# Kernel tuning notes

Measured on AMD Instinct MI355X. Metric: run time of the kernel, lower is better.

The kernel has to match this reference:

```python
import jax, jax.numpy as jnp
import numpy as np

B_, S_, H_, I_, N_, K_ = 2, 2048, 1024, 2048, 16, 4

def setup_inputs() -> dict:
    key = jax.random.key(0)
    ks = jax.random.split(key, 6)
    return {
        "x": jax.random.normal(ks[0], (B_, S_, H_), jnp.float32),
        "W_in": jax.random.normal(ks[1], (H_, 2 * I_), jnp.float32) * (H_ ** -0.5),
        "conv_w": jax.random.normal(ks[2], (I_, 1, K_), jnp.float32) * (K_ ** -0.5),
        "ln_gamma": jnp.ones((I_,), jnp.float32),
        "ln_beta": jnp.zeros((I_,), jnp.float32),
        "W_xproj": jax.random.normal(ks[3], (I_, 2 * N_ + 1), jnp.float32) * (I_ ** -0.5),
        "A_param": jax.random.normal(ks[4], (I_, N_), jnp.float32) * 0.1,
        "D": jnp.ones((I_,), jnp.float32),
        "W_out": jax.random.normal(ks[5], (I_, H_), jnp.float32) * (I_ ** -0.5),
    }

def _layernorm(x, g, b, eps=1e-5):
    mu = jnp.mean(x, axis=-1, keepdims=True)
    var = jnp.mean((x - mu) ** 2, axis=-1, keepdims=True)
    return (x - mu) * jax.lax.rsqrt(var + eps) * g + b

def reference(x, W_in, conv_w, ln_gamma, ln_beta, W_xproj, A_param, D, W_out):
    b, s, _ = x.shape
    n = A_param.shape[1]
    xz = x @ W_in                                   # (b,s,2I)
    xc, z = jnp.split(xz, 2, axis=-1)
    # depthwise causal conv1d: torch pads both sides k-1 then truncates [:s] == left-pad k-1
    xc = jax.lax.conv_general_dilated(
        xc.transpose(0, 2, 1), conv_w, window_strides=(1,),
        padding=[(conv_w.shape[-1] - 1, 0)],
        feature_group_count=conv_w.shape[0],
        dimension_numbers=("NCH", "OIH", "NCH")).transpose(0, 2, 1)  # (b,s,I)
    xc = jax.nn.silu(xc)
    xc = _layernorm(xc, ln_gamma, ln_beta)
    xp = xc @ W_xproj                               # (b,s,2N+1)
    delta = jnp.clip(jax.nn.softplus(xp[..., :1]), 1e-6, 10.0)   # (b,s,1)
    Bm = xp[..., 1:1 + n]                           # (b,s,N)
    Cm = xp[..., 1 + n:]                            # (b,s,N)
    A = -jnp.clip(jax.nn.softplus(A_param), 0.1, 10.0)           # (I,N)
    # decay[b,s,i,n] = exp(delta[b,s] * A[i,n]), clamped
    decay = jnp.clip(jnp.exp(delta[..., None] * A[None, None]), 1e-6, 1.0)  # (b,s,I,N)
    # y = x * sum_n B*C*decay  (state-dim reduction of the broadcast 4D tensor)
    y = xc * jnp.einsum("bsn,bsin->bsi", Bm * Cm, decay)
    y = y + xc * D
    return (y * jax.nn.silu(z)) @ W_out
```

## Files before the change

kernel.cpp:

```cpp
#include <hip/hip_runtime.h>
#include <hip/hip_bf16.h>
#include <cmath>

typedef __bf16 bf16_t;
typedef __bf16 bf16x8 __attribute__((ext_vector_type(8)));
typedef __bf16 bf16x4 __attribute__((ext_vector_type(4)));
typedef float  f32x4  __attribute__((ext_vector_type(4)));

static constexpr int B_  = 2, S_ = 2048, H_ = 1024, I_ = 2048, NST = 16;
static constexpr int ROWS  = B_ * S_;
static constexpr int TWO_I = 2 * I_;
static constexpr int XPD   = 2 * NST + 1;
static constexpr int XPN   = 64;

#define AS_G(p) ((const __attribute__((address_space(1))) void*)(p))
#define AS_L(p) ((__attribute__((address_space(3))) void*)(p))

template<int N> __device__ __forceinline__ void wait_vmcnt();
template<> __device__ __forceinline__ void wait_vmcnt<4>() {
    asm volatile("s_waitcnt vmcnt(4)" ::: "memory");
}

__device__ __forceinline__ float softplus_f(float x) {
    return x > 15.f ? x : log1pf(__expf(x));
}

__device__ __forceinline__ f32x4 b2f(bf16x4 v) {
    return (f32x4){(float)v[0], (float)v[1], (float)v[2], (float)v[3]};
}

__device__ __forceinline__ float fast_exp2(float x) {
#if __has_builtin(__builtin_amdgcn_exp2f)
    return __builtin_amdgcn_exp2f(x);
#else
    return exp2f(x);
#endif
}
__device__ __forceinline__ float fast_rcp(float x) {
#if __has_builtin(__builtin_amdgcn_rcpf)
    return __builtin_amdgcn_rcpf(x);
#else
    return 1.f / x;
#endif
}
__device__ __forceinline__ float fast_sigmoid(float x) {
    return fast_rcp(1.f + __expf(-x));
}
__device__ __forceinline__ float rflf(float x) {
    return __int_as_float(__builtin_amdgcn_readfirstlane(__float_as_int(x)));
}

template<int GX, int GY, int XW>
__device__ __forceinline__ void xcd_swz(int id, int& bx, int& by) {
    constexpr int SX = GX / XW;
    constexpr int SY = GY * XW / 8;
    const int xcd = id & 7;
    const int j   = id >> 3;
    bx = (xcd % XW) * SX + j % SX;
    by = (xcd / XW) * SY + j / SX;
}


__global__ __launch_bounds__(256)
void prep_all(const float* __restrict__ x, const float* __restrict__ W_in,
              const float* __restrict__ W_out, const float* __restrict__ A_param,
              const float* __restrict__ Wx, const float* __restrict__ conv_w,
              bf16_t* __restrict__ Xb, bf16_t* __restrict__ W1t,
              bf16_t* __restrict__ Wot, float* __restrict__ A2T,
              float* __restrict__ cwT, bf16_t* __restrict__ WxTb)
{
    const int b   = blockIdx.x;
    const int tid = threadIdx.x;
    __shared__ float t[32][33];

    if (b < 4096) {
        const int i = b * 256 + tid;
        f32x4 v = *(const f32x4*)(x + (size_t)i * 4);
        bf16x4 o;
        o[0] = (bf16_t)v[0]; o[1] = (bf16_t)v[1];
        o[2] = (bf16_t)v[2]; o[3] = (bf16_t)v[3];
        *(bf16x4*)(Xb + (size_t)i * 4) = o;
    } else if (b < 8192) {
        const int tb = b - 4096;
        const int c0 = (tb & 127) * 32, r0 = (tb >> 7) * 32;
        const int tx = tid & 31, ty = tid >> 5;
        #pragma unroll
        for (int k = 0; k < 4; ++k)
            t[ty + 8 * k][tx] = W_in[(size_t)(r0 + ty + 8 * k) * 4096 + c0 + tx];
        __syncthreads();
        #pragma unroll
        for (int k = 0; k < 4; ++k)
            W1t[(size_t)(c0 + ty + 8 * k) * 1024 + r0 + tx] = (bf16_t)t[tx][ty + 8 * k];
    } else if (b < 10240) {
        const int tb = b - 8192;
        const int c0 = (tb & 31) * 32, r0 = (tb >> 5) * 32;
        const int tx = tid & 31, ty = tid >> 5;
        #pragma unroll
        for (int k = 0; k < 4; ++k)
            t[ty + 8 * k][tx] = W_out[(size_t)(r0 + ty + 8 * k) * 1024 + c0 + tx];
        __syncthreads();
        #pragma unroll
        for (int k = 0; k < 4; ++k)
            Wot[(size_t)(c0 + ty + 8 * k) * 2048 + r0 + tx] = (bf16_t)t[tx][ty + 8 * k];
    } else {
        const int i = (b - 10240) * 256 + tid;
        if (i < NST * I_) {
            int n = i >> 11, c = i & (I_ - 1);
            float sp = softplus_f(A_param[(size_t)c * NST + n]);
            A2T[i] = -fminf(fmaxf(sp, 0.1f), 10.f) * 1.44269504088896340736f;
        }
        if (i < 4 * I_) {
            int j = i >> 11, c = i & (I_ - 1);
            cwT[i] = conv_w[(size_t)c * 4 + j];
        }
        if (i < XPN * I_) {
            int j = i >> 11, c = i & (I_ - 1);
            WxTb[i] = (j < XPD) ? (bf16_t)Wx[(size_t)c * XPD + j] : (bf16_t)0.f;
        }
    }
}


template<int M, int N, int K, int BM, int BN, int WM, int WN, int THREADS,
         int GX, int GY, int XW, typename OutT>
__global__ __launch_bounds__(THREADS)
void gemm_fp(const bf16_t* __restrict__ A, const bf16_t* __restrict__ Bt,
             OutT* __restrict__ C)
{
    constexpr int BK  = 32;
    constexpr int NT  = K / BK;
    constexpr int MR  = BM / WM / 16;
    constexpr int NR  = BN / WN / 16;
    constexpr int MH  = MR / 2;
    constexpr int RPC = THREADS / 4;
    constexpr int CA  = BM / RPC;
    constexpr int CB  = BN / RPC;
    static_assert(CA + CB == 4, "vmcnt template fixed at 4");

    __shared__ bf16_t lA[4][BM * BK];
    __shared__ bf16_t lB[4][BN * BK];

    int bx, by;
    xcd_swz<GX, GY, XW>(blockIdx.x, bx, by);
    const int bm = by * BM;
    const int bn = bx * BN;

    const int tid  = threadIdx.x;
    const int lane = tid & 63;
    const int wave = tid >> 6;
    const int wm   = wave / WN;
    const int wn   = wave % WN;

    const int frow = lane & 15;
    const int fsw  = ((lane >> 4) ^ ((frow >> 1) & 3)) << 3;

    const int str = tid >> 2;
    const int stp = tid & 3;

    const bf16_t* baseA[CA];
    #pragma unroll
    for (int a = 0; a < CA; ++a) {
        const int rt = a * RPC + str;
        baseA[a] = A + (size_t)(bm + rt) * K + ((stp ^ ((rt >> 1) & 3)) << 3);
    }
    const bf16_t* baseB[CB];
    #pragma unroll
    for (int a = 0; a < CB; ++a) {
        const int rt = a * RPC + str;
        baseB[a] = Bt + (size_t)(bn + rt) * K + ((stp ^ ((rt >> 1) & 3)) << 3);
    }

    f32x4 acc[MR][NR];
    #pragma unroll
    for (int m = 0; m < MR; ++m)
        #pragma unroll
        for (int n = 0; n < NR; ++n)
            acc[m][n] = (f32x4){0.f, 0.f, 0.f, 0.f};

    auto stageA = [&](int k0, int b) {
        #pragma unroll
        for (int a = 0; a < CA; ++a)
            __builtin_amdgcn_global_load_lds(AS_G(baseA[a] + k0),
                AS_L(&lA[b][a * RPC * 32 + wave * 512]), 16, 0, 0);
    };
    auto stageB = [&](int k0, int b) {
        #pragma unroll
        for (int a = 0; a < CB; ++a)
            __builtin_amdgcn_global_load_lds(AS_G(baseB[a] + k0),
                AS_L(&lB[b][a * RPC * 32 + wave * 512]), 16, 0, 0);
    };

    stageA(0, 0); stageB(0, 0);
    stageA(BK, 1); stageB(BK, 1);
    wait_vmcnt<4>();
    __builtin_amdgcn_s_barrier();

    #pragma unroll 1
    for (int t = 0; t < NT; ++t) {
        const int buf = t & 3;
        const int nb  = (t + 2) & 3;
        int kn = (t + 2) * BK;
        if (kn >= K) kn -= K;

        bf16x8 bfr[NR];
        #pragma unroll
        for (int n = 0; n < NR; ++n)
            bfr[n] = *(const bf16x8*)(&lB[buf][(wn * (NR * 16) + n * 16 + frow) * 32 + fsw]);
        bf16x8 af0[MH];
        #pragma unroll
        for (int m = 0; m < MH; ++m)
            af0[m] = *(const bf16x8*)(&lA[buf][(wm * (MR * 16) + m * 16 + frow) * 32 + fsw]);
        stageA(kn, nb);

        __builtin_amdgcn_s_setprio(1);
        #pragma unroll
        for (int m = 0; m < MH; ++m)
            #pragma unroll
            for (int n = 0; n < NR; ++n)
                acc[m][n] = __builtin_amdgcn_mfma_f32_16x16x32_bf16(
                    af0[m], bfr[n], acc[m][n], 0, 0, 0);
        __builtin_amdgcn_s_setprio(0);

        bf16x8 af1[MR - MH];
        #pragma unroll
        for (int m = 0; m < MR - MH; ++m)
            af1[m] = *(const bf16x8*)(&lA[buf][(wm * (MR * 16) + (MH + m) * 16 + frow) * 32 + fsw]);
        stageB(kn, nb);

        __builtin_amdgcn_s_setprio(1);
        #pragma unroll
        for (int m = 0; m < MR - MH; ++m)
            #pragma unroll
            for (int n = 0; n < NR; ++n)
                acc[MH + m][n] = __builtin_amdgcn_mfma_f32_16x16x32_bf16(
                    af1[m], bfr[n], acc[MH + m][n], 0, 0, 0);
        __builtin_amdgcn_s_setprio(0);

        wait_vmcnt<4>();
        __builtin_amdgcn_s_barrier();
    }

    const int crow = (lane >> 4) * 4;
    const int ccol = lane & 15;
    #pragma unroll
    for (int m = 0; m < MR; ++m)
        #pragma unroll
        for (int n = 0; n < NR; ++n)
            #pragma unroll
            for (int r = 0; r < 4; ++r)
                C[(size_t)(bm + wm * (MR * 16) + m * 16 + crow + r) * N
                  + (bn + wn * (NR * 16) + n * 16 + ccol)] = (OutT)acc[m][n][r];
}


template<int M, int N, int K, int GX, int GY, int XW>
__global__ __launch_bounds__(512)
void gemm3_kg(const bf16_t* __restrict__ A, const bf16_t* __restrict__ Bt,
              float* __restrict__ C)
{
    constexpr int BM = 128, BN = 128, BK = 32;
    constexpr int KH = K / 2;
    constexpr int NT = KH / BK;
    constexpr int MR = 4, NR = 4, MH = 2;

    __shared__ bf16_t smem[65536];

    int bx, by;
    xcd_swz<GX, GY, XW>(blockIdx.x, bx, by);
    const int bm = by * BM;
    const int bn = bx * BN;

    const int tid  = threadIdx.x;
    const int lane = tid & 63;
    const int wave = tid >> 6;
    const int grp  = wave >> 2;
    const int gw   = wave & 3;
    const int wm   = gw >> 1;
    const int wn   = gw & 1;

    const int frow = lane & 15;
    const int fsw  = ((lane >> 4) ^ ((frow >> 1) & 3)) << 3;

    const int gtid = tid & 255;
    const int str  = gtid >> 2;
    const int stp  = gtid & 3;

    bf16_t* lA = smem + grp * 16384;
    bf16_t* lB = smem + 32768 + grp * 16384;

    const bf16_t* baseA[2];
    #pragma unroll
    for (int a = 0; a < 2; ++a) {
        const int rt = a * 64 + str;
        baseA[a] = A + (size_t)(bm + rt) * K + grp * KH + ((stp ^ ((rt >> 1) & 3)) << 3);
    }
    const bf16_t* baseB[2];
    #pragma unroll
    for (int a = 0; a < 2; ++a) {
        const int rt = a * 64 + str;
        baseB[a] = Bt + (size_t)(bn + rt) * K + grp * KH + ((stp ^ ((rt >> 1) & 3)) << 3);
    }

    f32x4 acc[MR][NR];
    #pragma unroll
    for (int m = 0; m < MR; ++m)
        #pragma unroll
        for (int n = 0; n < NR; ++n)
            acc[m][n] = (f32x4){0.f, 0.f, 0.f, 0.f};

    auto stageA = [&](int k0, int b) {
        #pragma unroll
        for (int a = 0; a < 2; ++a)
            __builtin_amdgcn_global_load_lds(AS_G(baseA[a] + k0),
                AS_L(lA + b * 4096 + a * 2048 + gw * 512), 16, 0, 0);
    };
    auto stageB = [&](int k0, int b) {
        #pragma unroll
        for (int a = 0; a < 2; ++a)
            __builtin_amdgcn_global_load_lds(AS_G(baseB[a] + k0),
                AS_L(lB + b * 4096 + a * 2048 + gw * 512), 16, 0, 0);
    };

    stageA(0, 0); stageB(0, 0);
    stageA(BK, 1); stageB(BK, 1);
    wait_vmcnt<4>();
    __builtin_amdgcn_s_barrier();

    #pragma unroll 1
    for (int t = 0; t < NT; ++t) {
        const int buf = t & 3;
        const int nb  = (t + 2) & 3;
        int kn = (t + 2) * BK;
        if (kn >= KH) kn -= KH;

        bf16x8 bfr[NR];
        #pragma unroll
        for (int n = 0; n < NR; ++n)
            bfr[n] = *(const bf16x8*)(lB + buf * 4096 + (wn * 64 + n * 16 + frow) * 32 + fsw);
        bf16x8 af0[MH];
        #pragma unroll
        for (int m = 0; m < MH; ++m)
            af0[m] = *(const bf16x8*)(lA + buf * 4096 + (wm * 64 + m * 16 + frow) * 32 + fsw);
        stageA(kn, nb);

        __builtin_amdgcn_s_setprio(1);
        #pragma unroll
        for (int m = 0; m < MH; ++m)
            #pragma unroll
            for (int n = 0; n < NR; ++n)
                acc[m][n] = __builtin_amdgcn_mfma_f32_16x16x32_bf16(
                    af0[m], bfr[n], acc[m][n], 0, 0, 0);
        __builtin_amdgcn_s_setprio(0);

        bf16x8 af1[MR - MH];
        #pragma unroll
        for (int m = 0; m < MR - MH; ++m)
            af1[m] = *(const bf16x8*)(lA + buf * 4096 + (wm * 64 + (MH + m) * 16 + frow) * 32 + fsw);
        stageB(kn, nb);

        __builtin_amdgcn_s_setprio(1);
        #pragma unroll
        for (int m = 0; m < MR - MH; ++m)
            #pragma unroll
            for (int n = 0; n < NR; ++n)
                acc[MH + m][n] = __builtin_amdgcn_mfma_f32_16x16x32_bf16(
                    af1[m], bfr[n], acc[MH + m][n], 0, 0, 0);
        __builtin_amdgcn_s_setprio(0);

        wait_vmcnt<4>();
        __builtin_amdgcn_s_barrier();
    }

    asm volatile("s_waitcnt vmcnt(0)" ::: "memory");
    __builtin_amdgcn_s_barrier();

    float* accx = (float*)smem;
    const int crow = (lane >> 4) * 4;
    const int ccol = lane & 15;

    if (grp == 1) {
        #pragma unroll
        for (int m = 0; m < MR; ++m)
            #pragma unroll
            for (int n = 0; n < NR; ++n) {
                const int row = wm * 64 + m * 16 + crow;
                const int col = wn * 64 + n * 16 + ccol;
                #pragma unroll
                for (int r = 0; r < 4; ++r)
                    accx[(size_t)(row + r) * 132 + col] = acc[m][n][r];
            }
    }
    __syncthreads();
    if (grp == 0) {
        #pragma unroll
        for (int m = 0; m < MR; ++m)
            #pragma unroll
            for (int n = 0; n < NR; ++n) {
                const int row = wm * 64 + m * 16 + crow;
                const int col = wn * 64 + n * 16 + ccol;
                #pragma unroll
                for (int r = 0; r < 4; ++r)
                    C[(size_t)(bm + row + r) * N + bn + col] =
                        acc[m][n][r] + accx[(size_t)(row + r) * 132 + col];
            }
    }
}


__global__ __launch_bounds__(256)
void conv_ln(const bf16_t* __restrict__ xz,
             const float* __restrict__ cwT,
             const float* __restrict__ ln_g,
             const float* __restrict__ ln_b,
             bf16_t* __restrict__ Xn)
{
    const int row  = blockIdx.x;
    const int s    = row & (S_ - 1);
    const int tid  = threadIdx.x;
    const int lane = tid & 63;
    const int wave = tid >> 6;
    const bf16_t* xzr = xz + (size_t)row * TWO_I;

    __shared__ float lnr[4][2];

    float xc[8];
    float sm = 0.f, sq = 0.f;

    #pragma unroll
    for (int g = 0; g < 2; ++g) {
        const int c = g * 1024 + tid * 4;
        const f32x4 w0 = *(const f32x4*)(cwT + 0 * I_ + c);
        const f32x4 w1 = *(const f32x4*)(cwT + 1 * I_ + c);
        const f32x4 w2 = *(const f32x4*)(cwT + 2 * I_ + c);
        const f32x4 w3 = *(const f32x4*)(cwT + 3 * I_ + c);
        const f32x4 z4 = (f32x4){0.f, 0.f, 0.f, 0.f};
        const f32x4 xv0 = (s >= 3) ? b2f(*(const bf16x4*)(xzr - 3 * TWO_I + c)) : z4;
        const f32x4 xv1 = (s >= 2) ? b2f(*(const bf16x4*)(xzr - 2 * TWO_I + c)) : z4;
        const f32x4 xv2 = (s >= 1) ? b2f(*(const bf16x4*)(xzr - 1 * TWO_I + c)) : z4;
        const f32x4 xv3 = b2f(*(const bf16x4*)(xzr + c));
        const f32x4 a = w0 * xv0 + w1 * xv1 + w2 * xv2 + w3 * xv3;
        #pragma unroll
        for (int e = 0; e < 4; ++e) {
            const float v = a[e];
            const float t = v * fast_sigmoid(v);
            xc[g * 4 + e] = t;
            sm += t; sq += t * t;
        }
    }

    #pragma unroll
    for (int off = 32; off; off >>= 1) {
        sm += __shfl_xor(sm, off, 64);
        sq += __shfl_xor(sq, off, 64);
    }
    if (lane == 0) { lnr[wave][0] = sm; lnr[wave][1] = sq; }
    __syncthreads();
    sm = lnr[0][0] + lnr[1][0] + lnr[2][0] + lnr[3][0];
    sq = lnr[0][1] + lnr[1][1] + lnr[2][1] + lnr[3][1];
    const float mu = sm * (1.f / I_);
    const float rs = rsqrtf(sq * (1.f / I_) - mu * mu + 1e-5f);

    #pragma unroll
    for (int g = 0; g < 2; ++g) {
        const int c = g * 1024 + tid * 4;
        const f32x4 gg = *(const f32x4*)(ln_g + c);
        const f32x4 bb = *(const f32x4*)(ln_b + c);
        bf16x4 h4;
        #pragma unroll
        for (int e = 0; e < 4; ++e)
            h4[e] = (bf16_t)((xc[g * 4 + e] - mu) * rs * gg[e] + bb[e]);
        *(bf16x4*)(Xn + (size_t)row * I_ + c) = h4;
    }
}


__global__ __launch_bounds__(256)
void xproj_gemm(const bf16_t* __restrict__ Xn,
                const bf16_t* __restrict__ Wb, float* __restrict__ xp_part)
{
    constexpr int BM = 128, BK = 32, KS = 512;
    __shared__ bf16_t lA[BM * BK];
    __shared__ bf16_t lB[XPN * BK];

    const int bm   = blockIdx.x * BM;
    const int ks   = blockIdx.y;
    const int tid  = threadIdx.x;
    const int lane = tid & 63;
    const int wave = tid >> 6;
    const int wm   = (wave >> 1) * 64;
    const int wn   = (wave & 1) * 32;

    const int srow  = lane >> 2;
    const int skoff = (lane & 3) * 8;
    const int frow  = lane & 15;
    const int fko   = (lane >> 4) * 8;

    f32x4 acc[4][2];
    #pragma unroll
    for (int m = 0; m < 4; ++m)
        #pragma unroll
        for (int n = 0; n < 2; ++n)
            acc[m][n] = (f32x4){0.f, 0.f, 0.f, 0.f};

    for (int k0 = ks * KS; k0 < ks * KS + KS; k0 += BK) {
        #pragma unroll
        for (int t = 0; t < 2; ++t) {
            const int c = wave * 2 + t;
            const bf16_t* ga = Xn + (size_t)(bm + c * 16 + srow) * I_ + k0 + skoff;
            __builtin_amdgcn_global_load_lds(AS_G(ga), AS_L(lA + c * 512), 16, 0, 0);
        }
        const bf16_t* gb = Wb + (size_t)(wave * 16 + srow) * I_ + k0 + skoff;
        __builtin_amdgcn_global_load_lds(AS_G(gb), AS_L(lB + wave * 512), 16, 0, 0);
        __syncthreads();

        bf16x8 af[4], bf2[2];
        #pragma unroll
        for (int m = 0; m < 4; ++m)
            af[m] = *(const bf16x8*)(lA + (wm + m * 16 + frow) * BK + fko);
        #pragma unroll
        for (int n = 0; n < 2; ++n)
            bf2[n] = *(const bf16x8*)(lB + (wn + n * 16 + frow) * BK + fko);

        #pragma unroll
        for (int m = 0; m < 4; ++m)
            #pragma unroll
            for (int n = 0; n < 2; ++n)
                acc[m][n] = __builtin_amdgcn_mfma_f32_16x16x32_bf16(
                    af[m], bf2[n], acc[m][n], 0, 0, 0);

        __syncthreads();
    }

    float* out = xp_part + ((size_t)ks * ROWS + bm) * XPN;
    const int crow = (lane >> 4) * 4;
    const int ccol = lane & 15;
    #pragma unroll
    for (int m = 0; m < 4; ++m)
        #pragma unroll
        for (int n = 0; n < 2; ++n)
            #pragma unroll
            for (int r = 0; r < 4; ++r)
                out[(size_t)(wm + m * 16 + crow + r) * XPN
                    + (wn + n * 16 + ccol)] = acc[m][n][r];
}


__global__ __launch_bounds__(256)
void ssm_gate(const bf16_t* __restrict__ xz,
              const bf16_t* __restrict__ Xn,
              const float* __restrict__ xp_part,
              const float* __restrict__ A2T,
              const float* __restrict__ Dv,
              bf16_t* __restrict__ U)
{
    const int row0 = blockIdx.x * 2;
    const int tid  = threadIdx.x;

    __shared__ float xps[2][XPD];
    __shared__ float bcs[2][NST];

    if (tid < XPD) {
        float s = 0.f;
        #pragma unroll
        for (int ks = 0; ks < 4; ++ks)
            s += xp_part[((size_t)ks * ROWS + row0) * XPN + tid];
        xps[0][tid] = s;
    } else if (tid >= 64 && tid < 64 + XPD) {
        const int j = tid - 64;
        float s = 0.f;
        #pragma unroll
        for (int ks = 0; ks < 4; ++ks)
            s += xp_part[((size_t)ks * ROWS + row0 + 1) * XPN + j];
        xps[1][j] = s;
    }
    __syncthreads();
    if (tid < NST)
        bcs[0][tid] = xps[0][1 + tid] * xps[0][1 + NST + tid];
    else if (tid >= 64 && tid < 64 + NST) {
        const int n = tid - 64;
        bcs[1][n] = xps[1][1 + n] * xps[1][1 + NST + n];
    }
    __syncthreads();

    const float d0 = fminf(fmaxf(softplus_f(xps[0][0]), 1e-6f), 10.f);
    const float d1 = fminf(fmaxf(softplus_f(xps[1][0]), 1e-6f), 10.f);

    const bf16_t* z0 = xz + (size_t)row0 * TWO_I + I_;
    const bf16_t* z1 = z0 + TWO_I;
    bf16_t* u0 = U + (size_t)row0 * I_;
    bf16_t* u1 = u0 + I_;

    #pragma unroll 1
    for (int g = 0; g < 2; ++g) {
        const int c = g * 1024 + tid * 4;
        f32x4 sa0 = (f32x4){0.f, 0.f, 0.f, 0.f};
        f32x4 sa1 = (f32x4){0.f, 0.f, 0.f, 0.f};
        #pragma unroll 1
        for (int nb = 0; nb < 4; ++nb) {
            const float* ap = A2T + (size_t)(nb * 4) * I_ + c;
            const f32x4 a0 = *(const f32x4*)(ap);
            const f32x4 a1 = *(const f32x4*)(ap + I_);
            const f32x4 a2 = *(const f32x4*)(ap + 2 * I_);
            const f32x4 a3 = *(const f32x4*)(ap + 3 * I_);
            const float b00 = rflf(bcs[0][nb * 4 + 0]), b10 = rflf(bcs[1][nb * 4 + 0]);
            const float b01 = rflf(bcs[0][nb * 4 + 1]), b11 = rflf(bcs[1][nb * 4 + 1]);
            const float b02 = rflf(bcs[0][nb * 4 + 2]), b12 = rflf(bcs[1][nb * 4 + 2]);
            const float b03 = rflf(bcs[0][nb * 4 + 3]), b13 = rflf(bcs[1][nb * 4 + 3]);
            #pragma unroll
            for (int e = 0; e < 4; ++e) {
                sa0[e] += b00 * fast_exp2(d0 * a0[e]);
                sa1[e] += b10 * fast_exp2(d1 * a0[e]);
                sa0[e] += b01 * fast_exp2(d0 * a1[e]);
                sa1[e] += b11 * fast_exp2(d1 * a1[e]);
                sa0[e] += b02 * fast_exp2(d0 * a2[e]);
                sa1[e] += b12 * fast_exp2(d1 * a2[e]);
                sa0[e] += b03 * fast_exp2(d0 * a3[e]);
                sa1[e] += b13 * fast_exp2(d1 * a3[e]);
            }
        }
        const f32x4 dvv = *(const f32x4*)(Dv + c);
        const f32x4 xn0 = b2f(*(const bf16x4*)(Xn + (size_t)row0 * I_ + c));
        const f32x4 xn1 = b2f(*(const bf16x4*)(Xn + (size_t)(row0 + 1) * I_ + c));
        const f32x4 zv0 = b2f(*(const bf16x4*)(z0 + c));
        const f32x4 zv1 = b2f(*(const bf16x4*)(z1 + c));
        bf16x4 o0, o1;
        #pragma unroll
        for (int e = 0; e < 4; ++e) {
            const float y0 = xn0[e] * (sa0[e] + dvv[e]);
            const float y1 = xn1[e] * (sa1[e] + dvv[e]);
            const float zz0 = zv0[e], zz1 = zv1[e];
            o0[e] = (bf16_t)(y0 * zz0 * fast_sigmoid(zz0));
            o1[e] = (bf16_t)(y1 * zz1 * fast_sigmoid(zz1));
        }
        *(bf16x4*)(u0 + c) = o0;
        *(bf16x4*)(u1 + c) = o1;
    }
}


extern "C" void kernel_launch(void* const* d_in, const int* in_sizes, int n_in,
                              void* d_out, int out_size, void* d_ws, size_t ws_size,
                              hipStream_t stream)
{
    const float* x     = (const float*)d_in[0];
    const float* W_in  = (const float*)d_in[1];
    const float* convw = (const float*)d_in[2];
    const float* ln_g  = (const float*)d_in[3];
    const float* ln_b  = (const float*)d_in[4];
    const float* Wx    = (const float*)d_in[5];
    const float* A_p   = (const float*)d_in[6];
    const float* Dv    = (const float*)d_in[7];
    const float* W_out = (const float*)d_in[8];
    float* out = (float*)d_out;

    char* ws = (char*)d_ws;
    bf16_t* Xb   = (bf16_t*)(ws);
    bf16_t* W1t  = (bf16_t*)(ws + (size_t)(8u  << 20));
    bf16_t* Wot  = (bf16_t*)(ws + (size_t)(16u << 20));
    float*  A2T  = (float*) (ws + (size_t)(20u << 20));
    float*  cwT  = (float*) (ws + (size_t)(20u << 20) + (128u << 10));
    bf16_t* WxTb = (bf16_t*)(ws + (size_t)(20u << 20) + (256u << 10));
    bf16_t* XZb  = (bf16_t*)(ws + (size_t)(22u << 20));
    bf16_t* U    = (bf16_t*)(ws + (size_t)(54u << 20));
    bf16_t* Xn   = (bf16_t*)(ws);
    float*  xp4  = (float*) (ws + (size_t)(86u << 20));

    prep_all<<<10752, 256, 0, stream>>>(x, W_in, W_out, A_p, Wx, convw,
                                        Xb, W1t, Wot, A2T, cwT, WxTb);

    gemm_fp<ROWS, TWO_I, H_, 256, 256, 2, 4, 512, 16, 16, 4, bf16_t>
        <<<256, 512, 0, stream>>>(Xb, W1t, XZb);
    conv_ln<<<ROWS, 256, 0, stream>>>(XZb, cwT, ln_g, ln_b, Xn);
    xproj_gemm<<<dim3(ROWS / 128, 4), 256, 0, stream>>>(Xn, WxTb, xp4);
    ssm_gate<<<ROWS / 2, 256, 0, stream>>>(XZb, Xn, xp4, A2T, Dv, U);
    gemm3_kg<ROWS, H_, I_, 8, 32, 2>
        <<<256, 512, 0, stream>>>(U, Wot, out);
}
```

Baseline: 125.0 us.

## Rewrite input GEMM with BK=64 double-buffered eight-phase MFMA schedule

Replaces the generic four-buffer BK=32 GEMM for the input projection with a specialized 256x256 tile kernel using BK=64, two LDS buffers and a row-XOR swizzle over eight 16-byte chunks. Each K-tile is split into four MFMA quadrants separated by barriers, with fragment loads and global-to-LDS staging interleaved between them, to overlap memory with compute and cut per-iteration loop overhead. The added barriers and larger per-wave fragment register footprint may reduce latency hiding or occupancy. There is also a risk of LDS overwrite hazards when staging into the buffer currently being read.

```diff
diff --git a/kernel.cpp b/kernel.cpp
--- a/kernel.cpp
+++ b/kernel.cpp
@@ -19,6 +19,9 @@
 template<int N> __device__ __forceinline__ void wait_vmcnt();
 template<> __device__ __forceinline__ void wait_vmcnt<4>() {
     asm volatile("s_waitcnt vmcnt(4)" ::: "memory");
+}
+template<> __device__ __forceinline__ void wait_vmcnt<8>() {
+    asm volatile("s_waitcnt vmcnt(8)" ::: "memory");
 }
 
 __device__ __forceinline__ float softplus_f(float x) {
@@ -121,24 +124,17 @@
 }
 
 
-template<int M, int N, int K, int BM, int BN, int WM, int WN, int THREADS,
-         int GX, int GY, int XW, typename OutT>
-__global__ __launch_bounds__(THREADS)
-void gemm_fp(const bf16_t* __restrict__ A, const bf16_t* __restrict__ Bt,
-             OutT* __restrict__ C)
+template<int M, int N, int K, int GX, int GY, int XW>
+__global__ __launch_bounds__(512)
+void gemm1_8p(const bf16_t* __restrict__ A, const bf16_t* __restrict__ Bt,
+              bf16_t* __restrict__ C)
 {
-    constexpr int BK  = 32;
-    constexpr int NT  = K / BK;
-    constexpr int MR  = BM / WM / 16;
-    constexpr int NR  = BN / WN / 16;
-    constexpr int MH  = MR / 2;
-    constexpr int RPC = THREADS / 4;
-    constexpr int CA  = BM / RPC;
-    constexpr int CB  = BN / RPC;
-    static_assert(CA + CB == 4, "vmcnt template fixed at 4");
-
-    __shared__ bf16_t lA[4][BM * BK];
-    __shared__ bf16_t lB[4][BN * BK];
+    constexpr int BM = 256, BN = 256, BK = 64;
+    constexpr int NKT = K / BK;
+    constexpr int NIT = NKT / 2;
+
+    __shared__ bf16_t lA[2 * 16384];
+    __shared__ bf16_t lB[2 * 16384];
 
     int bx, by;
     xcd_swz<GX, GY, XW>(blockIdx.x, bx, by);
@@ -148,108 +144,162 @@
     const int tid  = threadIdx.x;
     const int lane = tid & 63;
     const int wave = tid >> 6;
-    const int wm   = wave / WN;
-    const int wn   = wave % WN;
-
+    const int wm   = wave >> 2;
+    const int wn   = wave & 3;
     const int frow = lane & 15;
-    const int fsw  = ((lane >> 4) ^ ((frow >> 1) & 3)) << 3;
-
-    const int str = tid >> 2;
-    const int stp = tid & 3;
-
-    const bf16_t* baseA[CA];
-    #pragma unroll
-    for (int a = 0; a < CA; ++a) {
-        const int rt = a * RPC + str;
-        baseA[a] = A + (size_t)(bm + rt) * K + ((stp ^ ((rt >> 1) & 3)) << 3);
-    }
-    const bf16_t* baseB[CB];
-    #pragma unroll
-    for (int a = 0; a < CB; ++a) {
-        const int rt = a * RPC + str;
-        baseB[a] = Bt + (size_t)(bn + rt) * K + ((stp ^ ((rt >> 1) & 3)) << 3);
-    }
-
-    f32x4 acc[MR][NR];
-    #pragma unroll
-    for (int m = 0; m < MR; ++m)
-        #pragma unroll
-        for (int n = 0; n < NR; ++n)
+    const int ko   = lane >> 4;
+    const int fr7  = frow & 7;
+
+    const int str = tid >> 3;
+    const int stp = tid & 7;
+
+    const bf16_t* gA[4];
+    const bf16_t* gB[4];
+    #pragma unroll
+    for (int h = 0; h < 2; ++h)
+        #pragma unroll
+        for (int a = 0; a < 2; ++a) {
+            const int rt = h * 128 + a * 64 + str;
+            gA[h * 2 + a] = A  + (size_t)(bm + rt) * K + ((stp ^ (str & 7)) << 3);
+            gB[h * 2 + a] = Bt + (size_t)(bn + rt) * K + ((stp ^ (str & 7)) << 3);
+        }
+    const int ldst = wave * 512;
+
+    f32x4 acc[8][4];
+    #pragma unroll
+    for (int m = 0; m < 8; ++m)
+        #pragma unroll
+        for (int n = 0; n < 4; ++n)
             acc[m][n] = (f32x4){0.f, 0.f, 0.f, 0.f};
 
-    auto stageA = [&](int k0, int b) {
-        #pragma unroll
-        for (int a = 0; a < CA; ++a)
-            __builtin_amdgcn_global_load_lds(AS_G(baseA[a] + k0),
-                AS_L(&lA[b][a * RPC * 32 + wave * 512]), 16, 0, 0);
+    auto stageA2 = [&](int kt, int buf) {
+        #pragma unroll
+        for (int c = 0; c < 4; ++c)
+            __builtin_amdgcn_global_load_lds(AS_G(gA[c] + kt * BK),
+                AS_L(lA + buf * 16384 + c * 4096 + ldst), 16, 0, 0);
     };
-    auto stageB = [&](int k0, int b) {
-        #pragma unroll
-        for (int a = 0; a < CB; ++a)
-            __builtin_amdgcn_global_load_lds(AS_G(baseB[a] + k0),
-                AS_L(&lB[b][a * RPC * 32 + wave * 512]), 16, 0, 0);
+    auto stageB2 = [&](int kt, int buf) {
+        #pragma unroll
+        for (int c = 0; c < 4; ++c)
+            __builtin_amdgcn_global_load_lds(AS_G(gB[c] + kt * BK),
+                AS_L(lB + buf * 16384 + c * 4096 + ldst), 16, 0, 0);
     };
 
-    stageA(0, 0); stageB(0, 0);
-    stageA(BK, 1); stageB(BK, 1);
-    wait_vmcnt<4>();
+    stageA2(0, 0); stageB2(0, 0);
+    stageA2(1, 1); stageB2(1, 1);
+    wait_vmcnt<8>();
     __builtin_amdgcn_s_barrier();
 
     #pragma unroll 1
-    for (int t = 0; t < NT; ++t) {
-        const int buf = t & 3;
-        const int nb  = (t + 2) & 3;
-        int kn = (t + 2) * BK;
-        if (kn >= K) kn -= K;
-
-        bf16x8 bfr[NR];
-        #pragma unroll
-        for (int n = 0; n < NR; ++n)
-            bfr[n] = *(const bf16x8*)(&lB[buf][(wn * (NR * 16) + n * 16 + frow) * 32 + fsw]);
-        bf16x8 af0[MH];
-        #pragma unroll
-        for (int m = 0; m < MH; ++m)
-            af0[m] = *(const bf16x8*)(&lA[buf][(wm * (MR * 16) + m * 16 + frow) * 32 + fsw]);
-        stageA(kn, nb);
-
-        __builtin_amdgcn_s_setprio(1);
-        #pragma unroll
-        for (int m = 0; m < MH; ++m)
-            #pragma unroll
-            for (int n = 0; n < NR; ++n)
-                acc[m][n] = __builtin_amdgcn_mfma_f32_16x16x32_bf16(
-                    af0[m], bfr[n], acc[m][n], 0, 0, 0);
-        __builtin_amdgcn_s_setprio(0);
-
-        bf16x8 af1[MR - MH];
-        #pragma unroll
-        for (int m = 0; m < MR - MH; ++m)
-            af1[m] = *(const bf16x8*)(&lA[buf][(wm * (MR * 16) + (MH + m) * 16 + frow) * 32 + fsw]);
-        stageB(kn, nb);
-
-        __builtin_amdgcn_s_setprio(1);
-        #pragma unroll
-        for (int m = 0; m < MR - MH; ++m)
-            #pragma unroll
-            for (int n = 0; n < NR; ++n)
-                acc[MH + m][n] = __builtin_amdgcn_mfma_f32_16x16x32_bf16(
-                    af1[m], bfr[n], acc[MH + m][n], 0, 0, 0);
-        __builtin_amdgcn_s_setprio(0);
-
-        wait_vmcnt<4>();
-        __builtin_amdgcn_s_barrier();
+    for (int it = 0; it < NIT; ++it) {
+        #pragma unroll
+        for (int half = 0; half < 2; ++half) {
+            const int buf = half;
+            const bf16_t* bufA = lA + buf * 16384;
+            const bf16_t* bufB = lB + buf * 16384;
+            int ktn = 2 * it + 2 + half;
+            if (ktn >= NKT) ktn -= NKT;
+
+            bf16x8 aF[8][2];
+            bf16x8 bF[2][2];
+
+            #pragma unroll
+            for (int m = 0; m < 4; ++m)
+                #pragma unroll
+                for (int kh = 0; kh < 2; ++kh)
+                    aF[m][kh] = *(const bf16x8*)(bufA + (wm * 128 + m * 16 + frow) * 64
+                                                 + ((((kh << 2) | ko) ^ fr7) << 3));
+            #pragma unroll
+            for (int n = 0; n < 2; ++n)
+                #pragma unroll
+                for (int kh = 0; kh < 2; ++kh)
+                    bF[n][kh] = *(const bf16x8*)(bufB + (wn * 64 + n * 16 + frow) * 64
+                                                 + ((((kh << 2) | ko) ^ fr7) << 3));
+            __builtin_amdgcn_s_barrier();
+            asm volatile("s_waitcnt lgkmcnt(0)" ::: "memory");
+            __builtin_amdgcn_sched_barrier(0);
+            __builtin_amdgcn_s_setprio(1);
+            #pragma unroll
+            for (int m = 0; m < 4; ++m)
+                #pragma unroll
+                for (int n = 0; n < 2; ++n)
+                    #pragma unroll
+                    for (int kh = 0; kh < 2; ++kh)
+                        acc[m][n] = __builtin_amdgcn_mfma_f32_16x16x32_bf16(
+                            aF[m][kh], bF[n][kh], acc[m][n], 0, 0, 0);
+            __builtin_amdgcn_s_setprio(0);
+            __builtin_amdgcn_s_barrier();
+
+            #pragma unroll
+            for (int m = 0; m < 4; ++m)
+                #pragma unroll
+                for (int kh = 0; kh < 2; ++kh)
+                    aF[4 + m][kh] = *(const bf16x8*)(bufA + (wm * 128 + (4 + m) * 16 + frow) * 64
+                                                     + ((((kh << 2) | ko) ^ fr7) << 3));
+            __builtin_amdgcn_s_barrier();
+            asm volatile("s_waitcnt lgkmcnt(0)" ::: "memory");
+            __builtin_amdgcn_sched_barrier(0);
+            __builtin_amdgcn_s_setprio(1);
+            #pragma unroll
+            for (int m = 0; m < 4; ++m)
+                #pragma unroll
+                for (int n = 0; n < 2; ++n)
+                    #pragma unroll
+                    for (int kh = 0; kh < 2; ++kh)
+                        acc[4 + m][n] = __builtin_amdgcn_mfma_f32_16x16x32_bf16(
+                            aF[4 + m][kh], bF[n][kh], acc[4 + m][n], 0, 0, 0);
+            __builtin_amdgcn_s_setprio(0);
+            __builtin_amdgcn_s_barrier();
+
+            #pragma unroll
+            for (int n = 0; n < 2; ++n)
+                #pragma unroll
+                for (int kh = 0; kh < 2; ++kh)
+                    bF[n][kh] = *(const bf16x8*)(bufB + (wn * 64 + (2 + n) * 16 + frow) * 64
+                                                 + ((((kh << 2) | ko) ^ fr7) << 3));
+            stageA2(ktn, buf);
+            __builtin_amdgcn_s_barrier();
+            asm volatile("s_waitcnt lgkmcnt(0)" ::: "memory");
+            __builtin_amdgcn_sched_barrier(0);
+            __builtin_amdgcn_s_setprio(1);
+            #pragma unroll
+            for (int m = 0; m < 4; ++m)
+                #pragma unroll
+                for (int n = 0; n < 2; ++n)
+                    #pragma unroll
+                    for (int kh = 0; kh < 2; ++kh)
+                        acc[m][2 + n] = __builtin_amdgcn_mfma_f32_16x16x32_bf16(
+                            aF[m][kh], bF[n][kh], acc[m][2 + n], 0, 0, 0);
+            __builtin_amdgcn_s_setprio(0);
+            __builtin_amdgcn_s_barrier();
+
+            stageB2(ktn, buf);
+            wait_vmcnt<8>();
+            __builtin_amdgcn_s_barrier();
+            __builtin_amdgcn_s_setprio(1);
+            #pragma unroll
+            for (int m = 0; m < 4; ++m)
+                #pragma unroll
+                for (int n = 0; n < 2; ++n)
+                    #pragma unroll
+                    for (int kh = 0; kh < 2; ++kh)
+                        acc[4 + m][2 + n] = __builtin_amdgcn_mfma_f32_16x16x32_bf16(
+                            aF[4 + m][kh], bF[n][kh], acc[4 + m][2 + n], 0, 0, 0);
+            __builtin_amdgcn_s_setprio(0);
+            __builtin_amdgcn_s_barrier();
+        }
     }
 
     const int crow = (lane >> 4) * 4;
     const int ccol = lane & 15;
     #pragma unroll
-    for (int m = 0; m < MR; ++m)
-        #pragma unroll
-        for (int n = 0; n < NR; ++n)
+    for (int m = 0; m < 8; ++m)
+        #pragma unroll
+        for (int n = 0; n < 4; ++n)
             #pragma unroll
             for (int r = 0; r < 4; ++r)
-                C[(size_t)(bm + wm * (MR * 16) + m * 16 + crow + r) * N
-                  + (bn + wn * (NR * 16) + n * 16 + ccol)] = (OutT)acc[m][n][r];
+                C[(size_t)(bm + wm * 128 + m * 16 + crow + r) * N
+                  + (bn + wn * 64 + n * 16 + ccol)] = (bf16_t)acc[m][n][r];
 }
 
 
@@ -668,7 +718,7 @@
     prep_all<<<10752, 256, 0, stream>>>(x, W_in, W_out, A_p, Wx, convw,
                                         Xb, W1t, Wot, A2T, cwT, WxTb);
 
-    gemm_fp<ROWS, TWO_I, H_, 256, 256, 2, 4, 512, 16, 16, 4, bf16_t>
+    gemm1_8p<ROWS, TWO_I, H_, 16, 16, 4>
         <<<256, 512, 0, stream>>>(Xb, W1t, XZb);
     conv_ln<<<ROWS, 256, 0, stream>>>(XZb, cwT, ln_g, ln_b, Xn);
     xproj_gemm<<<dim3(ROWS / 128, 4), 256, 0, stream>>>(Xn, WxTb, xp4);
```

Result: no change. 127.3 us (+1.8%).
